# Kernel optimization log

Measured on AMD Instinct MI355X. Metric: run time of the kernel, lower is better.

The kernel has to match this reference:

```python
import jax, jax.numpy as jnp
import numpy as np
import math

B, S, DM = 2, 1024, 1024
QH, KVH = 16, 4
DH = DM // QH            # 64
DHH = DH // 2            # 32
M = int(math.isqrt(S))   # 32
TOPK = 8
ROPE_BASE = 10000.0


def apply_rope(x):
    # x: [B, H, S, DH]; LLaMA-style rotary embedding, no freq scaling
    inv_freq = 1.0 / (ROPE_BASE ** (jnp.arange(0, DH, 2, dtype=jnp.float32) / DH))  # [DH/2]
    ang = jnp.arange(S, dtype=jnp.float32)[:, None] * inv_freq[None, :]             # [S, DH/2]
    cos = jnp.concatenate([jnp.cos(ang), jnp.cos(ang)], axis=-1)                    # [S, DH]
    sin = jnp.concatenate([jnp.sin(ang), jnp.sin(ang)], axis=-1)
    x1, x2 = x[..., :DHH], x[..., DHH:]
    rot = jnp.concatenate([-x2, x1], axis=-1)
    return x * cos[None, None] + rot * sin[None, None]


def gather_rows(src, idx):
    # src: [B, H, M, D], idx: [B, H, S, K] -> [B, H, S, K, D]
    return jnp.take_along_axis(src[:, :, None, :, :], idx[..., None], axis=3)


def setup_inputs() -> dict:
    key = jax.random.key(0)
    kx, kq, kk, kv, ko = jax.random.split(key, 5)
    std = 0.02
    return {
        "x": jax.random.normal(kx, (B, S, DM), dtype=jnp.float32),
        "wq": jax.random.normal(kq, (QH * DH, DM), dtype=jnp.float32) * std,
        "wk": jax.random.normal(kk, (KVH * DH, DM), dtype=jnp.float32) * std,
        "wv": jax.random.normal(kv, (KVH * DH, DM), dtype=jnp.float32) * std,
        "wo": jax.random.normal(ko, (DM, QH * DH), dtype=jnp.float32) * std,
    }


def reference(x, wq, wk, wv, wo):
    n_rep = QH // KVH
    q = (x @ wq.T).reshape(B, S, QH, DH).transpose(0, 2, 1, 3)    # [B,QH,S,DH]
    k = (x @ wk.T).reshape(B, S, KVH, DH).transpose(0, 2, 1, 3)   # [B,KVH,S,DH]
    v = (x @ wv.T).reshape(B, S, KVH, DH).transpose(0, 2, 1, 3)
    q = apply_rope(q)
    k = apply_rope(k)
    k = jnp.repeat(k, n_rep, axis=1)   # repeat_kv -> [B,QH,S,DH]
    v = jnp.repeat(v, n_rep, axis=1)

    k4 = k.reshape(B, QH, M, M, DH)
    k1 = k4[..., :DHH].sum(axis=-2)    # sum over columns -> [B,QH,M,DHH]
    k2 = k4[..., DHH:].sum(axis=-3)    # sum over rows    -> [B,QH,M,DHH]
    q1, q2 = q[..., :DHH], q[..., DHH:]

    # product-key candidate selection per half
    s1 = jnp.einsum('bhsd,bhmd->bhsm', q1, k1)
    _, idx1 = jax.lax.top_k(s1, TOPK)                              # [B,QH,S,K]
    vecs1 = gather_rows(k1, idx1)                                  # [B,QH,S,K,DHH]
    s2 = jnp.einsum('bhsd,bhmd->bhsm', q2, k2)
    _, idx2 = jax.lax.top_k(s2, TOPK)
    vecs2 = gather_rows(k2, idx2)

    # K x K cross product of candidate halves
    c1 = jnp.broadcast_to(vecs1[:, :, :, :, None, :], (B, QH, S, TOPK, TOPK, DHH))
    c2 = jnp.broadcast_to(vecs2[:, :, :, None, :, :], (B, QH, S, TOPK, TOPK, DHH))
    cand = jnp.concatenate([c1, c2], axis=-1).reshape(B, QH, S, TOPK * TOPK, DH)

    scores_final = jnp.einsum('bhsd,bhscd->bhsc', q, cand)
    _, sel = jax.lax.top_k(scores_final, TOPK)                     # [B,QH,S,K]
    final_k = jnp.take_along_axis(cand, sel[..., None], axis=3)    # [B,QH,S,K,DH]

    idx_in_k1 = sel // TOPK
    idx_in_k2 = sel % TOPK
    final_row = jnp.take_along_axis(idx1, idx_in_k1, axis=3)
    final_col = jnp.take_along_axis(idx2, idx_in_k2, axis=3)
    v_idx = final_row * M + final_col                              # [B,QH,S,K] in [0,S)
    final_v = gather_rows(v, v_idx)                                # [B,QH,S,K,DH]

    attn = jnp.einsum('bhsd,bhskd->bhsk', q, final_k) / math.sqrt(DH)
    w = jax.nn.softmax(attn, axis=-1)
    out = jnp.einsum('bhsk,bhskd->bhsd', w, final_v)               # [B,QH,S,DH]
    out = out.transpose(0, 2, 1, 3).reshape(B, S, QH * DH)
    return out @ wo.T
```

## Files before the change

### kernel.cpp

```cpp
#include <hip/hip_runtime.h>
#include <hip/hip_bf16.h>
#include <math.h>

constexpr int B_   = 2;
constexpr int S_   = 1024;
constexpr int DM_  = 1024;
constexpr int QH_  = 16;
constexpr int KVH_ = 4;
constexpr int DH_  = 64;
constexpr int DHH_ = 32;
constexpr int M_   = 32;
constexpr int TOPK_ = 8;
constexpr int BS_  = B_ * S_;
constexpr int NW_  = QH_*DH_ + 2*KVH_*DH_;
constexpr int KOFF_ = QH_*DH_;
constexpr int VOFF_ = KOFF_ + KVH_*DH_;

typedef __attribute__((ext_vector_type(8))) short short8v;
typedef __attribute__((ext_vector_type(4))) short short4v;
typedef __attribute__((ext_vector_type(4))) float float4v;

__device__ inline unsigned short bf16_rne(float f) {
    unsigned u = __float_as_uint(f);
    return (unsigned short)((u + 0x7FFFu + ((u >> 16) & 1u)) >> 16);
}
__device__ inline float bf16_back(unsigned short h) {
    return __uint_as_float(((unsigned)h) << 16);
}
__device__ __forceinline__ int swz(int srow) { return ((srow >> 1) & 3) << 4; }

__device__ __forceinline__ void gl_lds16(const void* g, void* l) {
    auto* gp = reinterpret_cast<const __attribute__((address_space(1))) unsigned int*>(
        reinterpret_cast<uintptr_t>(g));
    auto* lp = reinterpret_cast<__attribute__((address_space(3))) unsigned int*>(
        reinterpret_cast<uintptr_t>(l));
    __builtin_amdgcn_global_load_lds(gp, lp, 16, 0, 0);
}

template<int L>
__device__ __forceinline__ void split_banded(const float* __restrict__ src,
                                             int i, char* __restrict__ dst,
                                             int row0)
{
    float4 v = reinterpret_cast<const float4*>(src)[i];
    int row = row0 + (i >> 8);
    int col = (i & 255) << 2;
    int srow = row & 63;
    char* band = dst + (size_t)(row >> 6) * (32u * L * 4096u);
    int off = ((col >> 5) * L) * 4096 + srow * 64 +
              ((((col & 31) >> 3) * 16) ^ swz(srow)) + (col & 7) * 2;
    float f[4] = {v.x, v.y, v.z, v.w};
#pragma unroll
    for (int l = 0; l < L; ++l) {
        short4v s;
#pragma unroll
        for (int e = 0; e < 4; ++e) {
            unsigned short h = bf16_rne(f[e]);
            s[e] = (short)h;
            f[e] -= bf16_back(h);
        }
        *reinterpret_cast<short4v*>(band + off + l * 4096) = s;
    }
}

__global__ __launch_bounds__(256) void split_all_kernel(
    const float* __restrict__ x,  const float* __restrict__ wq,
    const float* __restrict__ wk, const float* __restrict__ wv,
    const float* __restrict__ wo,
    char* __restrict__ xs, char* __restrict__ wsp, char* __restrict__ wob)
{
    constexpr int E0 = BS_ * DM_ / 4;
    constexpr int E1 = E0 + KOFF_ * DM_ / 4;
    constexpr int E2 = E1 + (VOFF_ - KOFF_) * DM_ / 4;
    constexpr int E3 = E2 + (NW_ - VOFF_) * DM_ / 4;
    constexpr int E4 = E3 + DM_ * DM_ / 4;
    int i = blockIdx.x * 256 + threadIdx.x;
    if (i < E0)      split_banded<3>(x,  i,      xs,  0);
    else if (i < E1) split_banded<3>(wq, i - E0, wsp, 0);
    else if (i < E2) split_banded<3>(wk, i - E1, wsp, KOFF_);
    else if (i < E3) split_banded<3>(wv, i - E2, wsp, VOFF_);
    else if (i < E4) split_banded<1>(wo, i - E3, wob, 0);
}

template<int LEVELS>
__device__ __forceinline__ void stage_tile(const char* a, const char* b,
                                           char* AsB, char* BsB,
                                           int LA, int wvi, int lane)
{
#pragma unroll
    for (int l = 0; l < LEVELS; ++l) if (l < LA) {
        gl_lds16(a + l * 4096 + wvi * 1024 + lane * 16,
                 AsB + l * 4096 + wvi * 1024);
        gl_lds16(b + l * 4096 + wvi * 1024 + lane * 16,
                 BsB + l * 4096 + wvi * 1024);
    }
}

template<int LEVELS, int CROSS>
__global__ __launch_bounds__(256) void gemm_glds_kernel(
    const char* __restrict__ Aimg, const char* __restrict__ Bimg,
    int nVstart, float* __restrict__ C, int N, int K)
{
    __shared__ char As[2][LEVELS * 4096];
    __shared__ char Bs[2][LEVELS * 4096];
    const int tid = threadIdx.x;
    const int rowBase = blockIdx.x * 64;
    const int colBase = blockIdx.y * 64;
    const int lane = tid & 63, wvi = tid >> 6;
    const int wr = wvi >> 1, wc = wvi & 1;
    const int fr = lane & 15, fk = lane >> 4;
    const int LA = (colBase >= nVstart) ? 1 : LEVELS;

    const char* Ab = Aimg + (size_t)blockIdx.x * (32u * LEVELS * 4096u);
    const char* Bb = Bimg + (size_t)blockIdx.y * (32u * LEVELS * 4096u);

    float4v acc[2][2];
#pragma unroll
    for (int mi = 0; mi < 2; ++mi)
#pragma unroll
        for (int ni = 0; ni < 2; ++ni) acc[mi][ni] = (float4v)0.f;

    const int NKC = K >> 5;
    stage_tile<LEVELS>(Ab, Bb, &As[0][0], &Bs[0][0], LA, wvi, lane);
    __syncthreads();
    int buf = 0;
    for (int kc = 0; kc < NKC; ++kc) {
        if (kc + 1 < NKC)
            stage_tile<LEVELS>(Ab + (size_t)(kc + 1) * (LEVELS * 4096),
                               Bb + (size_t)(kc + 1) * (LEVELS * 4096),
                               &As[buf ^ 1][0], &Bs[buf ^ 1][0],
                               LA, wvi, lane);
        short8v aF[LEVELS][2];
#pragma unroll
        for (int l = 0; l < LEVELS; ++l) if (l < LA)
#pragma unroll
            for (int mi = 0; mi < 2; ++mi) {
                int row = wr * 32 + mi * 16 + fr;
                aF[l][mi] = *reinterpret_cast<const short8v*>(
                    &As[buf][l * 4096 + row * 64 + ((fk * 16) ^ swz(row))]);
            }
#pragma unroll
        for (int lb = 0; lb < LEVELS; ++lb) {
            if (lb >= LA) continue;
            short8v bF[2];
#pragma unroll
            for (int ni = 0; ni < 2; ++ni) {
                int row = wc * 32 + ni * 16 + fr;
                bF[ni] = *reinterpret_cast<const short8v*>(
                    &Bs[buf][lb * 4096 + row * 64 + ((fk * 16) ^ swz(row))]);
            }
#pragma unroll
            for (int la = 0; la < LEVELS; ++la) {
                if (la >= LA || la + lb > CROSS) continue;
#pragma unroll
                for (int mi = 0; mi < 2; ++mi)
#pragma unroll
                    for (int ni = 0; ni < 2; ++ni)
                        acc[mi][ni] = __builtin_amdgcn_mfma_f32_16x16x32_bf16(
                            aF[la][mi], bF[ni], acc[mi][ni], 0, 0, 0);
            }
        }
        __syncthreads();
        buf ^= 1;
    }
#pragma unroll
    for (int mi = 0; mi < 2; ++mi)
#pragma unroll
        for (int ni = 0; ni < 2; ++ni) {
            int row0 = rowBase + wr * 32 + mi * 16 + fk * 4;
            int col  = colBase + wc * 32 + ni * 16 + fr;
#pragma unroll
            for (int j = 0; j < 4; ++j)
                C[(size_t)(row0 + j) * N + col] = acc[mi][ni][j];
        }
}

template<int LEVELS, int CROSS>
__global__ __launch_bounds__(256) void gemm_mfma_kernel(
    const float* __restrict__ A,
    const float* __restrict__ W0, const float* __restrict__ W1,
    const float* __restrict__ W2, int n1, int n2,
    float* __restrict__ C, int N, int K)
{
    __shared__ short As[LEVELS * 64 * 32];
    __shared__ short Bs[LEVELS * 64 * 32];
    const int tid = threadIdx.x;
    const int rowBase = blockIdx.x * 64;
    const int colBase = blockIdx.y * 64;
    const int lane = tid & 63, wvi = tid >> 6;
    const int wr = wvi >> 1, wc = wvi & 1;
    const int fr = lane & 15, fk = lane >> 4;

    const float* aptr[2]; const float* bptr[2];
    int arow_[2], ac4_[2];
#pragma unroll
    for (int i = 0; i < 2; ++i) {
        int q = i * 256 + tid;
        int row = q >> 3, c4 = q & 7;
        arow_[i] = row; ac4_[i] = c4;
        aptr[i] = A + (size_t)(rowBase + row) * K + c4 * 4;
        int n = colBase + row;
        const float* wrow = (n < n1) ? W0 + (size_t)n * K
                          : (n < n2) ? W1 + (size_t)(n - n1) * K
                                     : W2 + (size_t)(n - n2) * K;
        bptr[i] = wrow + c4 * 4;
    }
    float4 pa[2], pb[2];
#pragma unroll
    for (int i = 0; i < 2; ++i) {
        pa[i] = *reinterpret_cast<const float4*>(aptr[i]);
        pb[i] = *reinterpret_cast<const float4*>(bptr[i]);
    }
    float4v acc[2][2];
#pragma unroll
    for (int mi = 0; mi < 2; ++mi)
#pragma unroll
        for (int ni = 0; ni < 2; ++ni) acc[mi][ni] = (float4v)0.f;

    const int NKC = K >> 5;
    for (int kc = 0; kc < NKC; ++kc) {
#pragma unroll
        for (int i = 0; i < 2; ++i) {
            int row = arow_[i];
            int base = row * 64 + ((ac4_[i] * 8) ^ swz(row));
            float fa[4] = {pa[i].x, pa[i].y, pa[i].z, pa[i].w};
            float fb[4] = {pb[i].x, pb[i].y, pb[i].z, pb[i].w};
#pragma unroll
            for (int l = 0; l < LEVELS; ++l) {
                short4v sa, sb;
#pragma unroll
                for (int e = 0; e < 4; ++e) {
                    unsigned short ha = bf16_rne(fa[e]);
                    unsigned short hb = bf16_rne(fb[e]);
                    sa[e] = (short)ha; sb[e] = (short)hb;
                    fa[e] -= bf16_back(ha);
                    fb[e] -= bf16_back(hb);
                }
                *reinterpret_cast<short4v*>((char*)As + l * 4096 + base) = sa;
                *reinterpret_cast<short4v*>((char*)Bs + l * 4096 + base) = sb;
            }
        }
        __syncthreads();
        if (kc + 1 < NKC) {
#pragma unroll
            for (int i = 0; i < 2; ++i) {
                pa[i] = *reinterpret_cast<const float4*>(aptr[i] + (kc+1)*32);
                pb[i] = *reinterpret_cast<const float4*>(bptr[i] + (kc+1)*32);
            }
        }
        short8v aF[LEVELS][2];
#pragma unroll
        for (int l = 0; l < LEVELS; ++l)
#pragma unroll
            for (int mi = 0; mi < 2; ++mi) {
                int row = wr * 32 + mi * 16 + fr;
                aF[l][mi] = *reinterpret_cast<const short8v*>(
                    (const char*)As + l * 4096 + row * 64 + ((fk * 16) ^ swz(row)));
            }
#pragma unroll
        for (int lb = 0; lb < LEVELS; ++lb) {
            short8v bF[2];
#pragma unroll
            for (int ni = 0; ni < 2; ++ni) {
                int row = wc * 32 + ni * 16 + fr;
                bF[ni] = *reinterpret_cast<const short8v*>(
                    (const char*)Bs + lb * 4096 + row * 64 + ((fk * 16) ^ swz(row)));
            }
#pragma unroll
            for (int la = 0; la < LEVELS; ++la) {
                if (la + lb > CROSS) continue;
#pragma unroll
                for (int mi = 0; mi < 2; ++mi)
#pragma unroll
                    for (int ni = 0; ni < 2; ++ni)
                        acc[mi][ni] = __builtin_amdgcn_mfma_f32_16x16x32_bf16(
                            aF[la][mi], bF[ni], acc[mi][ni], 0, 0, 0);
            }
        }
        __syncthreads();
    }
#pragma unroll
    for (int mi = 0; mi < 2; ++mi)
#pragma unroll
        for (int ni = 0; ni < 2; ++ni) {
            int row0 = rowBase + wr * 32 + mi * 16 + fk * 4;
            int col  = colBase + wc * 32 + ni * 16 + fr;
#pragma unroll
            for (int j = 0; j < 4; ++j)
                C[(size_t)(row0 + j) * N + col] = acc[mi][ni][j];
        }
}

__global__ __launch_bounds__(256) void rope_kernel(float* __restrict__ qkv)
{
    int id = blockIdx.x * 256 + threadIdx.x;
    int d  = id & 31;
    int r  = id >> 5;
    int h  = r % (QH_ + KVH_);
    int bs = r / (QH_ + KVH_);
    int s  = bs & (S_ - 1);
    float* base = qkv + (size_t)bs * NW_ +
                  (h < QH_ ? h * DH_ : KOFF_ + (h - QH_) * DH_);
    double e = (double)d * (1.0 / 32.0);
    float pf = (float)pow(10000.0, e);
    float inv_freq = __fdiv_rn(1.0f, pf);
    float ang = __fmul_rn((float)s, inv_freq);
    double sn64, cs64;
    sincos((double)ang, &sn64, &cs64);
    float cs = (float)cs64;
    float sn = (float)sn64;
    float x1 = base[d];
    float x2 = base[d + DHH_];
    base[d]        = __fadd_rn(__fmul_rn(x1, cs), __fmul_rn(-x2, sn));
    base[d + DHH_] = __fadd_rn(__fmul_rn(x2, cs), __fmul_rn(x1, sn));
}

__global__ __launch_bounds__(256) void k1k2_kernel(
    const float* __restrict__ qkv, float* __restrict__ k1,
    float* __restrict__ k2)
{
    int blk   = blockIdx.x;
    int bkv   = blk >> 2;
    int chunk = blk & 3;
    int b = bkv >> 2, kv = bkv & 3;
    int tid = threadIdx.x;
    int d  = tid & 31;
    int m  = chunk * 8 + (tid >> 5);
    const float* kbase = qkv + (size_t)b * S_ * NW_ + KOFF_ + kv * DH_;
    double s1 = 0., s2 = 0.;
    for (int mc = 0; mc < M_; ++mc) {
        s1 += (double)kbase[(size_t)(m * M_ + mc) * NW_ + d];
        s2 += (double)kbase[(size_t)(mc * M_ + m) * NW_ + DHH_ + d];
    }
    k1[((b * KVH_ + kv) * M_ + m) * DHH_ + d] = (float)s1;
    k2[((b * KVH_ + kv) * M_ + m) * DHH_ + d] = (float)s2;
}

template<int OUTMODE>
__global__ __launch_bounds__(256) void select4_kernel(
    const float* __restrict__ qkv,
    const float* __restrict__ k1g, const float* __restrict__ k2g,
    void* __restrict__ aout)
{
    __shared__ float k1s[M_][DHH_ + 1];
    __shared__ float k2s[M_][DHH_ + 1];
    __shared__ float qs[16][DH_];

    const int tid = threadIdx.x;
    const int bh  = blockIdx.x >> 6;
    const int s0  = (blockIdx.x & 63) << 4;
    const int b   = bh >> 4;
    const int h   = bh & 15;
    const int kv  = h >> 2;

    const int kbase = (b * KVH_ + kv) * M_ * DHH_;
    for (int i = tid; i < M_ * DHH_; i += 256) {
        k1s[i >> 5][i & 31] = k1g[kbase + i];
        k2s[i >> 5][i & 31] = k2g[kbase + i];
    }
    for (int i = tid; i < 16 * DH_; i += 256) {
        int r = i >> 6;
        qs[r][i & 63] = qkv[(size_t)(b * S_ + s0 + r) * NW_ + h * DH_ + (i & 63)];
    }
    const int w = tid >> 6, lane = tid & 63;
    __syncthreads();

    const int m = lane & 31;
    const bool hi = lane >= 32;
    const float* krow = hi ? &k2s[m][0] : &k1s[m][0];
    const int qoff = hi ? DHH_ : 0;

    float v1[4]; int i1[4];
#pragma unroll
    for (int u = 0; u < 4; ++u) { v1[u] = 0.f; i1[u] = m; }
#pragma unroll
    for (int d = 0; d < DHH_; ++d) {
        float kd = krow[d];
#pragma unroll
        for (int u = 0; u < 4; ++u)
            v1[u] = fmaf(qs[w * 4 + u][qoff + d], kd, v1[u]);
    }

    const int l5 = lane & 31;
#pragma unroll
    for (int k = 2; k <= 32; k <<= 1) {
#pragma unroll
        for (int j = k >> 1; j > 0; j >>= 1) {
            float ov[4]; int oi[4];
#pragma unroll
            for (int u = 0; u < 4; ++u) {
                ov[u] = __shfl_xor(v1[u], j);
                oi[u] = __shfl_xor(i1[u], j);
            }
            const bool dirD  = ((l5 & k) == 0);
            const bool lower = ((lane & j) == 0);
#pragma unroll
            for (int u = 0; u < 4; ++u) {
                bool gt = (v1[u] > ov[u]) || (v1[u] == ov[u] && i1[u] < oi[u]);
                if (gt != (dirD == lower)) { v1[u] = ov[u]; i1[u] = oi[u]; }
            }
        }
    }

    float v2[4]; int c2[4];
#pragma unroll
    for (int u = 0; u < 4; ++u) {
        float av = __shfl(v1[u], lane >> 3);
        float bv = __shfl(v1[u], 32 + (lane & 7));
        v2[u] = av + bv; c2[u] = lane;
    }
#pragma unroll
    for (int k = 2; k <= 64; k <<= 1) {
#pragma unroll
        for (int j = k >> 1; j > 0; j >>= 1) {
            float ov[4]; int oc[4];
#pragma unroll
            for (int u = 0; u < 4; ++u) {
                ov[u] = __shfl_xor(v2[u], j);
                oc[u] = __shfl_xor(c2[u], j);
            }
            const bool dirD  = ((lane & k) == 0);
            const bool lower = ((lane & j) == 0);
#pragma unroll
            for (int u = 0; u < 4; ++u) {
                bool gt = (v2[u] > ov[u]) || (v2[u] == ov[u] && c2[u] < oc[u]);
                if (gt != (dirD == lower)) { v2[u] = ov[u]; c2[u] = oc[u]; }
            }
        }
    }

    const float* vbase = qkv + (size_t)b * S_ * NW_ + VOFF_ + kv * DH_ + lane;
#pragma unroll
    for (int u = 0; u < 4; ++u) {
        float vmax = __shfl(v2[u], 0);
        float e = (lane < 8) ? expf((v2[u] - vmax) * 0.125f) : 0.f;
        float sum = e;
#pragma unroll
        for (int msk = 1; msk <= 4; msk <<= 1) sum += __shfl_xor(sum, msk);
        float wn = e / sum;
        float o = 0.f;
#pragma unroll
        for (int t = 0; t < TOPK_; ++t) {
            float wt  = __shfl(wn, t);
            int   ct  = __shfl(c2[u], t);
            int   row = __shfl(i1[u], ct >> 3);
            int   col = __shfl(i1[u], 32 + (ct & 7));
            o = fmaf(wt, vbase[(size_t)(row * M_ + col) * NW_], o);
        }
        int orow = b * S_ + s0 + w * 4 + u;
        int ocol = h * DH_ + lane;
        if (OUTMODE == 1) {
            int srow = orow & 63;
            size_t byteoff = (size_t)(orow >> 6) * (32u * 4096u)
                           + (size_t)(ocol >> 5) * 4096 + srow * 64
                           + ((((ocol & 31) >> 3) * 16) ^ swz(srow))
                           + (ocol & 7) * 2;
            *reinterpret_cast<short*>((char*)aout + byteoff) = (short)bf16_rne(o);
        } else {
            ((float*)aout)[(size_t)orow * (QH_ * DH_) + ocol] = o;
        }
    }
}

extern "C" void kernel_launch(void* const* d_in, const int* in_sizes, int n_in,
                              void* d_out, int out_size, void* d_ws,
                              size_t ws_size, hipStream_t stream)
{
    const float* x  = (const float*)d_in[0];
    const float* wq = (const float*)d_in[1];
    const float* wk = (const float*)d_in[2];
    const float* wv = (const float*)d_in[3];
    const float* wo = (const float*)d_in[4];
    float* out = (float*)d_out;

    float* wsf = (float*)d_ws;
    float* qkv = wsf;
    float* k1  = qkv + (size_t)BS_ * NW_;
    float* k2  = k1 + B_ * KVH_ * M_ * DHH_;

    const bool fast = ws_size >= 40960000ull;

    if (fast) {
        char* xs  = (char*)(k2 + B_ * KVH_ * M_ * DHH_);
        char* wsp = xs  + (size_t)3 * BS_ * DM_ * 2;
        char* wob = wsp + (size_t)3 * NW_ * DM_ * 2;
        char* aob = wob + (size_t)DM_ * DM_ * 2;

        constexpr int NSLOT = (BS_*DM_ + KOFF_*DM_ + (VOFF_-KOFF_)*DM_ +
                               (NW_-VOFF_)*DM_ + DM_*DM_) / 4;
        split_all_kernel<<<(NSLOT + 255) / 256, 256, 0, stream>>>(
            x, wq, wk, wv, wo, xs, wsp, wob);

        dim3 g1(BS_ / 64, NW_ / 64);
        gemm_glds_kernel<3, 2><<<g1, 256, 0, stream>>>(
            xs, wsp, VOFF_, qkv, NW_, DM_);
        rope_kernel<<<(BS_ * (QH_ + KVH_) * DHH_) / 256, 256, 0, stream>>>(qkv);
        k1k2_kernel<<<32, 256, 0, stream>>>(qkv, k1, k2);
        select4_kernel<1><<<B_ * QH_ * S_ / 16, 256, 0, stream>>>(
            qkv, k1, k2, aob);
        dim3 g2(BS_ / 64, DM_ / 64);
        gemm_glds_kernel<1, 0><<<g2, 256, 0, stream>>>(
            aob, wob, 1 << 30, out, DM_, DM_);
    } else {
        float* aout = k2 + B_ * KVH_ * M_ * DHH_;
        dim3 g1(BS_ / 64, NW_ / 64);
        gemm_mfma_kernel<3, 2><<<g1, 256, 0, stream>>>(
            x, wq, wk, wv, KOFF_, VOFF_, qkv, NW_, DM_);
        rope_kernel<<<(BS_ * (QH_ + KVH_) * DHH_) / 256, 256, 0, stream>>>(qkv);
        k1k2_kernel<<<32, 256, 0, stream>>>(qkv, k1, k2);
        select4_kernel<0><<<B_ * QH_ * S_ / 16, 256, 0, stream>>>(
            qkv, k1, k2, aout);
        dim3 g2(BS_ / 64, DM_ / 64);
        gemm_mfma_kernel<1, 0><<<g2, 256, 0, stream>>>(
            aout, wo, wo, wo, 1 << 30, 1 << 30, out, DM_, DM_);
    }
}
```

Before: 122.4 us.

## Replace warp bitonic top-k with per-thread insertion top-8 and pruned candidates

The selection kernel now assigns one query per thread. Each thread keeps the query in registers, computes the 32 half-scores per side, and keeps a running top-8 through an insertion network on packed double keys (score bits plus index). The 64-pair cross product is pruned to the 20 pairs that can reach the top 8 when both candidate lists are sorted. The V gather then goes through per-warp shared memory so lanes read contiguous output columns. This removes the shuffle-heavy bitonic sorts, but the grid shrinks to 256 blocks of 128 threads, which lowers occupancy and leaves more serial work per thread.

```diff
diff --git a/kernel.cpp b/kernel.cpp
--- a/kernel.cpp
+++ b/kernel.cpp
@@ -35,6 +35,29 @@
     auto* lp = reinterpret_cast<__attribute__((address_space(3))) unsigned int*>(
         reinterpret_cast<uintptr_t>(l));
     __builtin_amdgcn_global_load_lds(gp, lp, 16, 0, 0);
+}
+
+__device__ __forceinline__ double mkkey(float v, int idx) {
+    unsigned u = __float_as_uint(v);
+    unsigned s = u ^ ((unsigned)(((int)u) >> 31) | 0x80000000u);
+    return (double)s * 64.0 + (double)(63 - idx);
+}
+__device__ __forceinline__ void unkey(double kd, float& v, int& idx) {
+    double t = trunc(kd * 0.015625);
+    idx = 63 - (int)(kd - t * 64.0);
+    unsigned s = (unsigned)t;
+    unsigned u = s ^ (~((unsigned)(((int)s) >> 31)) | 0x80000000u);
+    v = __uint_as_float(u);
+}
+__device__ __forceinline__ void ins8(double* l, double x) {
+    l[7] = fmax(fmin(l[6], x), l[7]);
+    l[6] = fmax(fmin(l[5], x), l[6]);
+    l[5] = fmax(fmin(l[4], x), l[5]);
+    l[4] = fmax(fmin(l[3], x), l[4]);
+    l[3] = fmax(fmin(l[2], x), l[3]);
+    l[2] = fmax(fmin(l[1], x), l[2]);
+    l[1] = fmax(fmin(l[0], x), l[1]);
+    l[0] = fmax(x, l[0]);
 }
 
 template<int L>
@@ -337,117 +360,120 @@
 }
 
 template<int OUTMODE>
-__global__ __launch_bounds__(256) void select4_kernel(
+__global__ __launch_bounds__(128) void selectL_kernel(
     const float* __restrict__ qkv,
     const float* __restrict__ k1g, const float* __restrict__ k2g,
     void* __restrict__ aout)
 {
-    __shared__ float k1s[M_][DHH_ + 1];
-    __shared__ float k2s[M_][DHH_ + 1];
-    __shared__ float qs[16][DH_];
-
-    const int tid = threadIdx.x;
-    const int bh  = blockIdx.x >> 6;
-    const int s0  = (blockIdx.x & 63) << 4;
-    const int b   = bh >> 4;
-    const int h   = bh & 15;
-    const int kv  = h >> 2;
+    __shared__ __align__(16) float k1s[M_][DHH_];
+    __shared__ __align__(16) float k2s[M_][DHH_];
+    __shared__ float hof[2][64][33];
+    const int tid  = threadIdx.x;
+    const int bh   = blockIdx.x >> 3;
+    const int sblk = blockIdx.x & 7;
+    const int b    = bh >> 4;
+    const int h    = bh & 15;
+    const int kv   = h >> 2;
+    const int w    = tid >> 6, lane = tid & 63;
+    const int s    = sblk * 128 + w * 64 + lane;
 
     const int kbase = (b * KVH_ + kv) * M_ * DHH_;
-    for (int i = tid; i < M_ * DHH_; i += 256) {
+    for (int i = tid; i < M_ * DHH_; i += 128) {
         k1s[i >> 5][i & 31] = k1g[kbase + i];
         k2s[i >> 5][i & 31] = k2g[kbase + i];
     }
-    for (int i = tid; i < 16 * DH_; i += 256) {
-        int r = i >> 6;
-        qs[r][i & 63] = qkv[(size_t)(b * S_ + s0 + r) * NW_ + h * DH_ + (i & 63)];
-    }
-    const int w = tid >> 6, lane = tid & 63;
     __syncthreads();
 
-    const int m = lane & 31;
-    const bool hi = lane >= 32;
-    const float* krow = hi ? &k2s[m][0] : &k1s[m][0];
-    const int qoff = hi ? DHH_ : 0;
-
-    float v1[4]; int i1[4];
-#pragma unroll
-    for (int u = 0; u < 4; ++u) { v1[u] = 0.f; i1[u] = m; }
-#pragma unroll
-    for (int d = 0; d < DHH_; ++d) {
-        float kd = krow[d];
-#pragma unroll
-        for (int u = 0; u < 4; ++u)
-            v1[u] = fmaf(qs[w * 4 + u][qoff + d], kd, v1[u]);
-    }
-
-    const int l5 = lane & 31;
-#pragma unroll
-    for (int k = 2; k <= 32; k <<= 1) {
-#pragma unroll
-        for (int j = k >> 1; j > 0; j >>= 1) {
-            float ov[4]; int oi[4];
-#pragma unroll
-            for (int u = 0; u < 4; ++u) {
-                ov[u] = __shfl_xor(v1[u], j);
-                oi[u] = __shfl_xor(i1[u], j);
-            }
-            const bool dirD  = ((l5 & k) == 0);
-            const bool lower = ((lane & j) == 0);
-#pragma unroll
-            for (int u = 0; u < 4; ++u) {
-                bool gt = (v1[u] > ov[u]) || (v1[u] == ov[u] && i1[u] < oi[u]);
-                if (gt != (dirD == lower)) { v1[u] = ov[u]; i1[u] = oi[u]; }
-            }
-        }
-    }
-
-    float v2[4]; int c2[4];
-#pragma unroll
-    for (int u = 0; u < 4; ++u) {
-        float av = __shfl(v1[u], lane >> 3);
-        float bv = __shfl(v1[u], 32 + (lane & 7));
-        v2[u] = av + bv; c2[u] = lane;
-    }
-#pragma unroll
-    for (int k = 2; k <= 64; k <<= 1) {
-#pragma unroll
-        for (int j = k >> 1; j > 0; j >>= 1) {
-            float ov[4]; int oc[4];
-#pragma unroll
-            for (int u = 0; u < 4; ++u) {
-                ov[u] = __shfl_xor(v2[u], j);
-                oc[u] = __shfl_xor(c2[u], j);
-            }
-            const bool dirD  = ((lane & k) == 0);
-            const bool lower = ((lane & j) == 0);
-#pragma unroll
-            for (int u = 0; u < 4; ++u) {
-                bool gt = (v2[u] > ov[u]) || (v2[u] == ov[u] && c2[u] < oc[u]);
-                if (gt != (dirD == lower)) { v2[u] = ov[u]; c2[u] = oc[u]; }
-            }
-        }
-    }
+    const float* qrow = qkv + (size_t)(b * S_ + s) * NW_ + h * DH_;
+    float q[64];
+#pragma unroll
+    for (int i = 0; i < 16; ++i)
+        *reinterpret_cast<float4*>(&q[i * 4]) =
+            *reinterpret_cast<const float4*>(qrow + i * 4);
+
+    double l[8];
+    float av[8], bv[8];
+    int i1v[8], i2v[8];
+#pragma unroll
+    for (int p = 0; p < 8; ++p) l[p] = -1.0;
+    for (int m = 0; m < M_; ++m) {
+        float acc = 0.f;
+#pragma unroll
+        for (int d4 = 0; d4 < 8; ++d4) {
+            float4 k4 = *reinterpret_cast<const float4*>(&k1s[m][d4 * 4]);
+            acc = fmaf(q[d4 * 4 + 0], k4.x, acc);
+            acc = fmaf(q[d4 * 4 + 1], k4.y, acc);
+            acc = fmaf(q[d4 * 4 + 2], k4.z, acc);
+            acc = fmaf(q[d4 * 4 + 3], k4.w, acc);
+        }
+        ins8(l, mkkey(acc, m));
+    }
+#pragma unroll
+    for (int p = 0; p < 8; ++p) unkey(l[p], av[p], i1v[p]);
+#pragma unroll
+    for (int p = 0; p < 8; ++p) l[p] = -1.0;
+    for (int m = 0; m < M_; ++m) {
+        float acc = 0.f;
+#pragma unroll
+        for (int d4 = 0; d4 < 8; ++d4) {
+            float4 k4 = *reinterpret_cast<const float4*>(&k2s[m][d4 * 4]);
+            acc = fmaf(q[32 + d4 * 4 + 0], k4.x, acc);
+            acc = fmaf(q[32 + d4 * 4 + 1], k4.y, acc);
+            acc = fmaf(q[32 + d4 * 4 + 2], k4.z, acc);
+            acc = fmaf(q[32 + d4 * 4 + 3], k4.w, acc);
+        }
+        ins8(l, mkkey(acc, m));
+    }
+#pragma unroll
+    for (int p = 0; p < 8; ++p) unkey(l[p], bv[p], i2v[p]);
+
+#pragma unroll
+    for (int p = 0; p < 8; ++p) l[p] = -1.0;
+#define CAND(i, j) ins8(l, mkkey(av[i] + bv[j], (i) * 8 + (j)))
+    CAND(0,0); CAND(0,1); CAND(0,2); CAND(0,3);
+    CAND(0,4); CAND(0,5); CAND(0,6); CAND(0,7);
+    CAND(1,0); CAND(1,1); CAND(1,2); CAND(1,3);
+    CAND(2,0); CAND(2,1); CAND(3,0); CAND(3,1);
+    CAND(4,0); CAND(5,0); CAND(6,0); CAND(7,0);
+#undef CAND
+    float v2[8]; int c2[8];
+#pragma unroll
+    for (int p = 0; p < 8; ++p) unkey(l[p], v2[p], c2[p]);
+
+    float ex[8]; float sum = 0.f;
+#pragma unroll
+    for (int t = 0; t < 8; ++t) {
+        ex[t] = expf((v2[t] - v2[0]) * 0.125f);
+        sum += ex[t];
+    }
+    const float inv = 1.0f / sum;
+
+#pragma unroll
+    for (int p = 0; p < 8; ++p) {
+        hof[w][lane][p]     = __int_as_float(i1v[p]);
+        hof[w][lane][8 + p] = __int_as_float(i2v[p]);
+    }
+#pragma unroll
+    for (int t = 0; t < 8; ++t) {
+        int i = c2[t] >> 3, j = c2[t] & 7;
+        int row = __float_as_int(hof[w][lane][i]);
+        int col = __float_as_int(hof[w][lane][8 + j]);
+        hof[w][lane][16 + t] = ex[t] * inv;
+        hof[w][lane][24 + t] = __int_as_float(row * M_ + col);
+    }
+    __syncthreads();
 
     const float* vbase = qkv + (size_t)b * S_ * NW_ + VOFF_ + kv * DH_ + lane;
-#pragma unroll
-    for (int u = 0; u < 4; ++u) {
-        float vmax = __shfl(v2[u], 0);
-        float e = (lane < 8) ? expf((v2[u] - vmax) * 0.125f) : 0.f;
-        float sum = e;
-#pragma unroll
-        for (int msk = 1; msk <= 4; msk <<= 1) sum += __shfl_xor(sum, msk);
-        float wn = e / sum;
+#pragma unroll 4
+    for (int p = 0; p < 64; ++p) {
         float o = 0.f;
 #pragma unroll
-        for (int t = 0; t < TOPK_; ++t) {
-            float wt  = __shfl(wn, t);
-            int   ct  = __shfl(c2[u], t);
-            int   row = __shfl(i1[u], ct >> 3);
-            int   col = __shfl(i1[u], 32 + (ct & 7));
-            o = fmaf(wt, vbase[(size_t)(row * M_ + col) * NW_], o);
-        }
-        int orow = b * S_ + s0 + w * 4 + u;
+        for (int t = 0; t < 8; ++t) {
+            float wt = hof[w][p][16 + t];
+            int   vr = __float_as_int(hof[w][p][24 + t]);
+            o = fmaf(wt, vbase[(size_t)vr * NW_], o);
+        }
+        int orow = b * S_ + sblk * 128 + w * 64 + p;
         int ocol = h * DH_ + lane;
         if (OUTMODE == 1) {
             int srow = orow & 63;
@@ -496,7 +522,7 @@
             xs, wsp, VOFF_, qkv, NW_, DM_);
         rope_kernel<<<(BS_ * (QH_ + KVH_) * DHH_) / 256, 256, 0, stream>>>(qkv);
         k1k2_kernel<<<32, 256, 0, stream>>>(qkv, k1, k2);
-        select4_kernel<1><<<B_ * QH_ * S_ / 16, 256, 0, stream>>>(
+        selectL_kernel<1><<<B_ * QH_ * 8, 128, 0, stream>>>(
             qkv, k1, k2, aob);
         dim3 g2(BS_ / 64, DM_ / 64);
         gemm_glds_kernel<1, 0><<<g2, 256, 0, stream>>>(
@@ -508,7 +534,7 @@
             x, wq, wk, wv, KOFF_, VOFF_, qkv, NW_, DM_);
         rope_kernel<<<(BS_ * (QH_ + KVH_) * DHH_) / 256, 256, 0, stream>>>(qkv);
         k1k2_kernel<<<32, 256, 0, stream>>>(qkv, k1, k2);
-        select4_kernel<0><<<B_ * QH_ * S_ / 16, 256, 0, stream>>>(
+        selectL_kernel<0><<<B_ * QH_ * 8, 128, 0, stream>>>(
             qkv, k1, k2, aout);
         dim3 g2(BS_ / 64, DM_ / 64);
         gemm_mfma_kernel<1, 0><<<g2, 256, 0, stream>>>(
```

Result: slower. 136.1 us (+11.2%).
